# Performance work log

Measured on AMD Instinct MI355X. Metric: run time of the kernel, lower is better.

Reference implementation:

```python
import jax, jax.numpy as jnp
import numpy as np

NUM_QUERIES = 256  # num_queries init arg
D = 256            # decoder_dim


def fps(xyz, n):
    """Furthest point sampling, matching the CUDA furthest_point_sample kernel:
    start at index 0, keep running min squared distance, pick argmax each step.
    xyz: [B, N, 3] -> indices [B, n] int32."""
    B, N, _ = xyz.shape

    def step(carry, _):
        dist, far = carry
        centroid = jnp.take_along_axis(xyz, far[:, None, None], axis=1)  # [B,1,3]
        d = jnp.sum((xyz - centroid) ** 2, axis=-1)                      # [B,N]
        dist = jnp.minimum(dist, d)
        return (dist, jnp.argmax(dist, axis=-1).astype(jnp.int32)), far

    init = (jnp.full((B, N), 1e10, xyz.dtype), jnp.zeros((B,), jnp.int32))
    _, inds = jax.lax.scan(step, init, None, length=n)
    return jnp.transpose(inds)  # [B, n]


def setup_inputs() -> dict:
    key = jax.random.key(0)
    ks = jax.random.split(key, 6)
    B, N = 64, 32768
    # scene coords in roughly [-3, 3]^3 meters
    encoder_xyz = jax.random.uniform(ks[0], (B, N, 3), jnp.float32) * 6.0 - 3.0
    pc_min = jnp.min(encoder_xyz, axis=1)  # [B,3]
    pc_max = jnp.max(encoder_xyz, axis=1)  # [B,3]
    gauss_B = jax.random.normal(ks[1], (3, D // 2), jnp.float32)  # fourier freqs
    W1 = jax.random.normal(ks[2], (D, D), jnp.float32) / np.sqrt(D)
    b1 = jnp.zeros((D,), jnp.float32)
    W2 = jax.random.normal(ks[3], (D, D), jnp.float32) / np.sqrt(D)
    b2 = jnp.zeros((D,), jnp.float32)
    return dict(encoder_xyz=encoder_xyz, pc_min=pc_min, pc_max=pc_max,
                gauss_B=gauss_B, W1=W1, b1=b1, W2=W2, b2=b2)


def reference(encoder_xyz, pc_min, pc_max, gauss_B, W1, b1, W2, b2):
    # --- query selection: FPS + gather (indices are non-differentiable) ---
    inds = fps(jax.lax.stop_gradient(encoder_xyz), NUM_QUERIES)          # [B,nq]
    query_xyz = jnp.take_along_axis(encoder_xyz, inds[..., None], axis=1)  # [B,nq,3]
    # --- PositionEmbeddingCoordsSine (fourier, normalize=True) ---
    norm = (query_xyz - pc_min[:, None, :]) / (pc_max - pc_min)[:, None, :]
    proj = (2.0 * jnp.pi) * jnp.einsum('bnd,df->bnf', norm, gauss_B)     # [B,nq,D/2]
    pos = jnp.concatenate([jnp.sin(proj), jnp.cos(proj)], axis=-1)       # [B,nq,D]
    pos = jnp.transpose(pos, (0, 2, 1))                                   # [B,D,nq]
    # --- query_projection GenericMLP: conv1x1 + ReLU, conv1x1 + output ReLU ---
    h = jax.nn.relu(jnp.einsum('bcn,dc->bdn', pos, W1) + b1[:, None])
    query_embed = jax.nn.relu(jnp.einsum('bcn,dc->bdn', h, W2) + b2[:, None])
    return query_xyz, query_embed
```

## Files before the change

kernel.cpp:

```cpp
#include <hip/hip_runtime.h>

#define FPS_N 32768
#define FPS_T 256
#define NBLK 8
#define PPB (FPS_N / NBLK)
#define PPT (PPB / FPS_T)
#define NCH (PPT / 4)
#define NQ 256
#define DD 256
#define NT 64
#define B_BATCH 64

#define WS_CLEAR_BYTES (B_BATCH * NQ * NBLK * 8)

__global__ __attribute__((amdgpu_flat_work_group_size(FPS_T, FPS_T),
                          amdgpu_waves_per_eu(2, 2)))
void fps_kernel(const float* __restrict__ xyz, float* __restrict__ qout,
                unsigned long long* __restrict__ gslot) {
  const int gid = blockIdx.x;
  const int xcd = gid & 7;
  const int s = gid >> 3;
  const int b = xcd + 8 * (s >> 3);
  const int q = s & 7;
  const int t = threadIdx.x;

  const float* __restrict__ base = xyz + (size_t)b * (FPS_N * 3);
  const float4* __restrict__ base4 =
      (const float4*)(base + (size_t)q * PPB * 3) + (size_t)t * (PPT * 3 / 4);
  float* qb = qout + (size_t)b * (NQ * 3);
  unsigned long long* bslot = gslot + (size_t)b * (NQ * NBLK);

  __shared__ unsigned long long sred[FPS_T / 64];
  __shared__ float4 bc;

  float4 C[PPT * 3 / 4];
#pragma unroll
  for (int i = 0; i < PPT * 3 / 4; ++i) C[i] = base4[i];
#pragma unroll
  for (int i = 0; i < PPT * 3 / 4; ++i) {
    asm volatile("" : "+v"(C[i].x), "+v"(C[i].y), "+v"(C[i].z), "+v"(C[i].w));
  }
  float4 Dst[NCH];
#pragma unroll
  for (int c = 0; c < NCH; ++c) Dst[c] = make_float4(1e10f, 1e10f, 1e10f, 1e10f);

  if (q == 0 && t == 0) { qb[0] = base[0]; qb[1] = base[1]; qb[2] = base[2]; }
  float cx = base[0], cy = base[1], cz = base[2];

#pragma unroll 1
  for (int j = 1; j < NQ; ++j) {
    float best = -1.0f;
    int bik = 0;

#pragma unroll
    for (int c = 0; c < NCH; ++c) {
      const float4 a4 = C[3 * c + 0];
      const float4 b4 = C[3 * c + 1];
      const float4 c4 = C[3 * c + 2];
      const float px[4] = {a4.x, a4.w, b4.z, c4.y};
      const float py[4] = {a4.y, b4.x, b4.w, c4.z};
      const float pz[4] = {a4.z, b4.y, c4.x, c4.w};
      const float dold[4] = {Dst[c].x, Dst[c].y, Dst[c].z, Dst[c].w};
      float dnew[4];
#pragma unroll
      for (int i = 0; i < 4; ++i) {
        const float dx = __fsub_rn(px[i], cx);
        const float dy = __fsub_rn(py[i], cy);
        const float dz = __fsub_rn(pz[i], cz);
        const float d = __fadd_rn(__fadd_rn(__fmul_rn(dx, dx), __fmul_rn(dy, dy)),
                                  __fmul_rn(dz, dz));
        const float nd = fminf(dold[i], d);
        dnew[i] = nd;
        if (nd > best) { best = nd; bik = c * 4 + i; }
      }
      Dst[c] = make_float4(dnew[0], dnew[1], dnew[2], dnew[3]);
    }
    int bi = q * PPB + t * PPT + bik;

#pragma unroll
    for (int off = 32; off; off >>= 1) {
      const float ov = __shfl_xor(best, off);
      const int oi = __shfl_xor(bi, off);
      if (ov > best || (ov == best && oi < bi)) { best = ov; bi = oi; }
    }
    if ((t & 63) == 0) {
      sred[t >> 6] = ((unsigned long long)(unsigned int)__float_as_int(best) << 32) |
                     (unsigned int)~(unsigned int)bi;
    }
    __syncthreads();

    if (t < 64) {
      unsigned long long p = sred[t & 3];
#pragma unroll
      for (int off = 1; off < 4; off <<= 1) {
        const unsigned long long o = __shfl_xor(p, off);
        if (o > p) p = o;
      }
      if (t == 0) {
        __hip_atomic_store(&bslot[j * NBLK + q], p, __ATOMIC_RELAXED,
                           __HIP_MEMORY_SCOPE_AGENT);
      }
      unsigned long long rp = 0;
      if (t < NBLK) {
        do {
          rp = __hip_atomic_load(&bslot[j * NBLK + t], __ATOMIC_RELAXED,
                                 __HIP_MEMORY_SCOPE_AGENT);
        } while (rp == 0ull);
      }
#pragma unroll
      for (int off = 1; off < NBLK; off <<= 1) {
        const unsigned long long o = __shfl_xor(rp, off);
        if (o > rp) rp = o;
      }
      if (t == 0) {
        const int gi = (int)~(unsigned int)(rp & 0xffffffffull);
        const float* cp = base + 3 * (size_t)gi;
        const float ncx = cp[0], ncy = cp[1], ncz = cp[2];
        bc = make_float4(ncx, ncy, ncz, 0.f);
        if (q == 0) { qb[3 * j + 0] = ncx; qb[3 * j + 1] = ncy; qb[3 * j + 2] = ncz; }
      }
    }
    __syncthreads();
    cx = bc.x; cy = bc.y; cz = bc.z;
  }
}

__global__ __launch_bounds__(256) void embed_mlp_kernel(
    const float* __restrict__ qxyz, const float* __restrict__ pcmin,
    const float* __restrict__ pcmax, const float* __restrict__ G,
    const float* __restrict__ W1, const float* __restrict__ b1,
    const float* __restrict__ W2, const float* __restrict__ b2,
    float* __restrict__ out) {
  const int b = blockIdx.x >> 2;
  const int n0 = (blockIdx.x & 3) * NT;
  const int tid = threadIdx.x;
  const int ty = tid >> 4, tx = tid & 15;

  __shared__ __align__(16) float P[DD][NT + 4];
  __shared__ __align__(16) float H[DD][NT + 4];
  __shared__ __align__(16) float Wl[64][NT + 4];
  __shared__ float snorm[NT][3];

  if (tid < NT) {
    const int n = n0 + tid;
    const float qx = qxyz[(size_t)b * (NQ * 3) + 3 * n + 0];
    const float qy = qxyz[(size_t)b * (NQ * 3) + 3 * n + 1];
    const float qz = qxyz[(size_t)b * (NQ * 3) + 3 * n + 2];
    snorm[tid][0] = (qx - pcmin[3 * b + 0]) / (pcmax[3 * b + 0] - pcmin[3 * b + 0]);
    snorm[tid][1] = (qy - pcmin[3 * b + 1]) / (pcmax[3 * b + 1] - pcmin[3 * b + 1]);
    snorm[tid][2] = (qz - pcmin[3 * b + 2]) / (pcmax[3 * b + 2] - pcmin[3 * b + 2]);
  }
  __syncthreads();

  {
    const int nn = tid & 63;
    const int fg = tid >> 6;
    const float nx = snorm[nn][0], ny = snorm[nn][1], nz = snorm[nn][2];
#pragma unroll 4
    for (int ff = 0; ff < 32; ++ff) {
      const int f = fg * 32 + ff;
      const float s = nx * G[f] + ny * G[128 + f] + nz * G[256 + f];
      const float proj = 6.28318530717958647692f * s;
      P[f][nn] = sinf(proj);
      P[f + 128][nn] = cosf(proj);
    }
  }

  for (int layer = 0; layer < 2; ++layer) {
    const float* W = layer ? W2 : W1;
    const float* bias = layer ? b2 : b1;
    const float (*src)[NT + 4] = layer ? H : P;

    for (int dt = 0; dt < 4; ++dt) {
      float acc[4][4] = {};
      for (int kt = 0; kt < 4; ++kt) {
        __syncthreads();
        {
          const int r = tid >> 2;
          const int cb = (tid & 3) * 16;
          const float* wrow = W + (size_t)(dt * 64 + r) * DD + kt * 64 + cb;
#pragma unroll
          for (int i = 0; i < 4; ++i) {
            const float4 v = *(const float4*)(wrow + 4 * i);
            Wl[cb + 4 * i + 0][r] = v.x;
            Wl[cb + 4 * i + 1][r] = v.y;
            Wl[cb + 4 * i + 2][r] = v.z;
            Wl[cb + 4 * i + 3][r] = v.w;
          }
        }
        __syncthreads();
#pragma unroll 8
        for (int cc = 0; cc < 64; ++cc) {
          const float4 a = *(const float4*)&Wl[cc][ty * 4];
          const float4 p4 = *(const float4*)&src[kt * 64 + cc][tx * 4];
          acc[0][0] = fmaf(a.x, p4.x, acc[0][0]);
          acc[0][1] = fmaf(a.x, p4.y, acc[0][1]);
          acc[0][2] = fmaf(a.x, p4.z, acc[0][2]);
          acc[0][3] = fmaf(a.x, p4.w, acc[0][3]);
          acc[1][0] = fmaf(a.y, p4.x, acc[1][0]);
          acc[1][1] = fmaf(a.y, p4.y, acc[1][1]);
          acc[1][2] = fmaf(a.y, p4.z, acc[1][2]);
          acc[1][3] = fmaf(a.y, p4.w, acc[1][3]);
          acc[2][0] = fmaf(a.z, p4.x, acc[2][0]);
          acc[2][1] = fmaf(a.z, p4.y, acc[2][1]);
          acc[2][2] = fmaf(a.z, p4.z, acc[2][2]);
          acc[2][3] = fmaf(a.z, p4.w, acc[2][3]);
          acc[3][0] = fmaf(a.w, p4.x, acc[3][0]);
          acc[3][1] = fmaf(a.w, p4.y, acc[3][1]);
          acc[3][2] = fmaf(a.w, p4.z, acc[3][2]);
          acc[3][3] = fmaf(a.w, p4.w, acc[3][3]);
        }
      }
      if (layer == 0) {
#pragma unroll
        for (int i = 0; i < 4; ++i) {
          const float bv = bias[dt * 64 + ty * 4 + i];
          float4 h;
          h.x = fmaxf(acc[i][0] + bv, 0.f);
          h.y = fmaxf(acc[i][1] + bv, 0.f);
          h.z = fmaxf(acc[i][2] + bv, 0.f);
          h.w = fmaxf(acc[i][3] + bv, 0.f);
          *(float4*)&H[dt * 64 + ty * 4 + i][tx * 4] = h;
        }
      } else {
        float* ob = out + (size_t)b * (DD * NQ);
#pragma unroll
        for (int i = 0; i < 4; ++i) {
          const float bv = bias[dt * 64 + ty * 4 + i];
          float4 h;
          h.x = fmaxf(acc[i][0] + bv, 0.f);
          h.y = fmaxf(acc[i][1] + bv, 0.f);
          h.z = fmaxf(acc[i][2] + bv, 0.f);
          h.w = fmaxf(acc[i][3] + bv, 0.f);
          *(float4*)(ob + (size_t)(dt * 64 + ty * 4 + i) * NQ + n0 + tx * 4) = h;
        }
      }
    }
  }
}

extern "C" void kernel_launch(void* const* d_in, const int* in_sizes, int n_in,
                              void* d_out, int out_size, void* d_ws, size_t ws_size,
                              hipStream_t stream) {
  (void)in_sizes; (void)n_in; (void)ws_size; (void)out_size;
  const float* xyz   = (const float*)d_in[0];
  const float* pcmin = (const float*)d_in[1];
  const float* pcmax = (const float*)d_in[2];
  const float* G     = (const float*)d_in[3];
  const float* W1    = (const float*)d_in[4];
  const float* b1    = (const float*)d_in[5];
  const float* W2    = (const float*)d_in[6];
  const float* b2    = (const float*)d_in[7];

  float* qxyz  = (float*)d_out;
  float* embed = qxyz + (size_t)B_BATCH * NQ * 3;

  unsigned long long* gslot = (unsigned long long*)d_ws;

  hipMemsetAsync(d_ws, 0, WS_CLEAR_BYTES, stream);

  hipLaunchKernelGGL(fps_kernel, dim3(B_BATCH * NBLK), dim3(FPS_T), 0, stream,
                     xyz, qxyz, gslot);
  hipLaunchKernelGGL(embed_mlp_kernel, dim3(B_BATCH * 4), dim3(256), 0, stream,
                     qxyz, pcmin, pcmax, G, W1, b1, W2, b2, embed);
}
```

Before: 582.4 us.

## Carry winning point coordinates through FPS reductions to skip global centroid reload

Each thread now selects the coordinates of its best point from registers and carries them, along with the packed distance/index key, through the wave, block and cross-block reductions. Each block publishes three 64-bit slots (key, xy, z) instead of one. The final lane then reads the centroid from the reduced values rather than loading it from global memory after the reduction, taking a dependent global load off the serial per-iteration critical path. In exchange it adds register selection work, extra shuffles and triple the slot traffic, and switches the ready sentinel to all-ones with a 0xFF memset.

```diff
diff --git a/kernel.cpp b/kernel.cpp
--- a/kernel.cpp
+++ b/kernel.cpp
@@ -11,7 +11,8 @@
 #define NT 64
 #define B_BATCH 64
 
-#define WS_CLEAR_BYTES (B_BATCH * NQ * NBLK * 8)
+#define WS_CLEAR_BYTES (B_BATCH * NQ * NBLK * 3 * 8)
+#define SENT 0xffffffffffffffffull
 
 __global__ __attribute__((amdgpu_flat_work_group_size(FPS_T, FPS_T),
                           amdgpu_waves_per_eu(2, 2)))
@@ -23,14 +24,17 @@
   const int b = xcd + 8 * (s >> 3);
   const int q = s & 7;
   const int t = threadIdx.x;
+  const int w = t >> 6;
+  const int lane = t & 63;
 
   const float* __restrict__ base = xyz + (size_t)b * (FPS_N * 3);
   const float4* __restrict__ base4 =
       (const float4*)(base + (size_t)q * PPB * 3) + (size_t)t * (PPT * 3 / 4);
   float* qb = qout + (size_t)b * (NQ * 3);
-  unsigned long long* bslot = gslot + (size_t)b * (NQ * NBLK);
-
-  __shared__ unsigned long long sred[FPS_T / 64];
+  unsigned long long* bslot = gslot + ((size_t)b * NQ) * (NBLK * 3);
+
+  __shared__ unsigned long long redp[FPS_T / 64], redxy[FPS_T / 64];
+  __shared__ float redz[FPS_T / 64];
   __shared__ float4 bc;
 
   float4 C[PPT * 3 / 4];
@@ -75,49 +79,81 @@
       }
       Dst[c] = make_float4(dnew[0], dnew[1], dnew[2], dnew[3]);
     }
-    int bi = q * PPB + t * PPT + bik;
+    const int bi = q * PPB + t * PPT + bik;
+    unsigned long long p =
+        ((unsigned long long)(unsigned int)__float_as_int(best) << 32) |
+        (unsigned int)~(unsigned int)bi;
+
+    float wx = 0.f, wy = 0.f, wz = 0.f;
+#pragma unroll
+    for (int c = 0; c < NCH; ++c) {
+      const float4 a4 = C[3 * c + 0];
+      const float4 b4 = C[3 * c + 1];
+      const float4 c4 = C[3 * c + 2];
+      const float px[4] = {a4.x, a4.w, b4.z, c4.y};
+      const float py[4] = {a4.y, b4.x, b4.w, c4.z};
+      const float pz[4] = {a4.z, b4.y, c4.x, c4.w};
+#pragma unroll
+      for (int i = 0; i < 4; ++i) {
+        if (c * 4 + i == bik) { wx = px[i]; wy = py[i]; wz = pz[i]; }
+      }
+    }
+    unsigned long long pxy = ((unsigned long long)__float_as_uint(wy) << 32) |
+                             __float_as_uint(wx);
+    float pz2 = wz;
 
 #pragma unroll
     for (int off = 32; off; off >>= 1) {
-      const float ov = __shfl_xor(best, off);
-      const int oi = __shfl_xor(bi, off);
-      if (ov > best || (ov == best && oi < bi)) { best = ov; bi = oi; }
-    }
-    if ((t & 63) == 0) {
-      sred[t >> 6] = ((unsigned long long)(unsigned int)__float_as_int(best) << 32) |
-                     (unsigned int)~(unsigned int)bi;
-    }
+      const unsigned long long op = __shfl_xor(p, off);
+      const unsigned long long oxy = __shfl_xor(pxy, off);
+      const float oz = __shfl_xor(pz2, off);
+      if (op > p) { p = op; pxy = oxy; pz2 = oz; }
+    }
+    if (lane == 0) { redp[w] = p; redxy[w] = pxy; redz[w] = pz2; }
     __syncthreads();
 
-    if (t < 64) {
-      unsigned long long p = sred[t & 3];
-#pragma unroll
-      for (int off = 1; off < 4; off <<= 1) {
-        const unsigned long long o = __shfl_xor(p, off);
-        if (o > p) p = o;
-      }
-      if (t == 0) {
-        __hip_atomic_store(&bslot[j * NBLK + q], p, __ATOMIC_RELAXED,
-                           __HIP_MEMORY_SCOPE_AGENT);
-      }
-      unsigned long long rp = 0;
-      if (t < NBLK) {
+    if (w == 0) {
+      if (lane < 4) {
+        p = redp[lane]; pxy = redxy[lane]; pz2 = redz[lane];
+#pragma unroll
+        for (int off = 1; off < 4; off <<= 1) {
+          const unsigned long long op = __shfl_xor(p, off);
+          const unsigned long long oxy = __shfl_xor(pxy, off);
+          const float oz = __shfl_xor(pz2, off);
+          if (op > p) { p = op; pxy = oxy; pz2 = oz; }
+        }
+      }
+      if (lane == 0) {
+        unsigned long long* sl = bslot + (size_t)j * (NBLK * 3) + q * 3;
+        __hip_atomic_store(&sl[0], p, __ATOMIC_RELAXED, __HIP_MEMORY_SCOPE_AGENT);
+        __hip_atomic_store(&sl[1], pxy, __ATOMIC_RELAXED, __HIP_MEMORY_SCOPE_AGENT);
+        __hip_atomic_store(&sl[2], (unsigned long long)__float_as_uint(pz2),
+                           __ATOMIC_RELAXED, __HIP_MEMORY_SCOPE_AGENT);
+      }
+      unsigned long long own = 0;
+      if (lane < NBLK * 3) {
+        const unsigned long long* sl = bslot + (size_t)j * (NBLK * 3) + lane;
         do {
-          rp = __hip_atomic_load(&bslot[j * NBLK + t], __ATOMIC_RELAXED,
-                                 __HIP_MEMORY_SCOPE_AGENT);
-        } while (rp == 0ull);
-      }
+          own = __hip_atomic_load(sl, __ATOMIC_RELAXED, __HIP_MEMORY_SCOPE_AGENT);
+        } while (own == SENT);
+      }
+      const int l3 = lane * 3;
+      const unsigned long long gp = __shfl(own, l3);
+      const unsigned long long gxy = __shfl(own, l3 + 1);
+      const unsigned long long gz = __shfl(own, l3 + 2);
+      p = gp; pxy = gxy; pz2 = __uint_as_float((unsigned int)gz);
 #pragma unroll
       for (int off = 1; off < NBLK; off <<= 1) {
-        const unsigned long long o = __shfl_xor(rp, off);
-        if (o > rp) rp = o;
-      }
-      if (t == 0) {
-        const int gi = (int)~(unsigned int)(rp & 0xffffffffull);
-        const float* cp = base + 3 * (size_t)gi;
-        const float ncx = cp[0], ncy = cp[1], ncz = cp[2];
-        bc = make_float4(ncx, ncy, ncz, 0.f);
-        if (q == 0) { qb[3 * j + 0] = ncx; qb[3 * j + 1] = ncy; qb[3 * j + 2] = ncz; }
+        const unsigned long long op = __shfl_xor(p, off);
+        const unsigned long long oxy = __shfl_xor(pxy, off);
+        const float oz = __shfl_xor(pz2, off);
+        if (op > p) { p = op; pxy = oxy; pz2 = oz; }
+      }
+      if (lane == 0) {
+        const float ncx = __uint_as_float((unsigned int)(pxy & 0xffffffffull));
+        const float ncy = __uint_as_float((unsigned int)(pxy >> 32));
+        bc = make_float4(ncx, ncy, pz2, 0.f);
+        if (q == 0) { qb[3 * j + 0] = ncx; qb[3 * j + 1] = ncy; qb[3 * j + 2] = pz2; }
       }
     }
     __syncthreads();
@@ -257,7 +293,7 @@
 
   unsigned long long* gslot = (unsigned long long*)d_ws;
 
-  hipMemsetAsync(d_ws, 0, WS_CLEAR_BYTES, stream);
+  hipMemsetAsync(d_ws, 0xFF, WS_CLEAR_BYTES, stream);
 
   hipLaunchKernelGGL(fps_kernel, dim3(B_BATCH * NBLK), dim3(FPS_T), 0, stream,
                      xyz, qxyz, gslot);
```

Result: slower. 759.0 us (+30.3%).

## Drop second barrier per FPS step by having every wave poll cross-block slots

Applied to the files above, without the earlier changes.

Each FPS iteration now performs the intra-block reduction with a single packed 64-bit shuffle and a double-buffered shared slot. All four waves then redundantly do the final block combine and spin on the global per-block slots, and each loads the new centroid directly. This removes the second __syncthreads and the LDS broadcast of the centroid. The workspace sentinel changes from zero to all-ones so that a real packed value can never match it. The trade-off is four times as many polling loads on the global slots and redundant centroid loads per block.

```diff
diff --git a/kernel.cpp b/kernel.cpp
--- a/kernel.cpp
+++ b/kernel.cpp
@@ -12,6 +12,7 @@
 #define B_BATCH 64
 
 #define WS_CLEAR_BYTES (B_BATCH * NQ * NBLK * 8)
+#define SENT 0xffffffffffffffffull
 
 __global__ __attribute__((amdgpu_flat_work_group_size(FPS_T, FPS_T),
                           amdgpu_waves_per_eu(2, 2)))
@@ -23,6 +24,8 @@
   const int b = xcd + 8 * (s >> 3);
   const int q = s & 7;
   const int t = threadIdx.x;
+  const int w = t >> 6;
+  const int lane = t & 63;
 
   const float* __restrict__ base = xyz + (size_t)b * (FPS_N * 3);
   const float4* __restrict__ base4 =
@@ -30,8 +33,7 @@
   float* qb = qout + (size_t)b * (NQ * 3);
   unsigned long long* bslot = gslot + (size_t)b * (NQ * NBLK);
 
-  __shared__ unsigned long long sred[FPS_T / 64];
-  __shared__ float4 bc;
+  __shared__ unsigned long long sredp[2][4];
 
   float4 C[PPT * 3 / 4];
 #pragma unroll
@@ -75,53 +77,52 @@
       }
       Dst[c] = make_float4(dnew[0], dnew[1], dnew[2], dnew[3]);
     }
-    int bi = q * PPB + t * PPT + bik;
+    const int bi = q * PPB + t * PPT + bik;
+    unsigned long long p =
+        ((unsigned long long)(unsigned int)__float_as_int(best) << 32) |
+        (unsigned int)~(unsigned int)bi;
 
 #pragma unroll
     for (int off = 32; off; off >>= 1) {
-      const float ov = __shfl_xor(best, off);
-      const int oi = __shfl_xor(bi, off);
-      if (ov > best || (ov == best && oi < bi)) { best = ov; bi = oi; }
-    }
-    if ((t & 63) == 0) {
-      sred[t >> 6] = ((unsigned long long)(unsigned int)__float_as_int(best) << 32) |
-                     (unsigned int)~(unsigned int)bi;
-    }
+      const unsigned long long o = __shfl_xor(p, off);
+      if (o > p) p = o;
+    }
+    if (lane == 0) sredp[j & 1][w] = p;
     __syncthreads();
 
-    if (t < 64) {
-      unsigned long long p = sred[t & 3];
-#pragma unroll
-      for (int off = 1; off < 4; off <<= 1) {
-        const unsigned long long o = __shfl_xor(p, off);
-        if (o > p) p = o;
-      }
-      if (t == 0) {
-        __hip_atomic_store(&bslot[j * NBLK + q], p, __ATOMIC_RELAXED,
-                           __HIP_MEMORY_SCOPE_AGENT);
-      }
-      unsigned long long rp = 0;
-      if (t < NBLK) {
-        do {
-          rp = __hip_atomic_load(&bslot[j * NBLK + t], __ATOMIC_RELAXED,
-                                 __HIP_MEMORY_SCOPE_AGENT);
-        } while (rp == 0ull);
-      }
-#pragma unroll
-      for (int off = 1; off < NBLK; off <<= 1) {
-        const unsigned long long o = __shfl_xor(rp, off);
-        if (o > rp) rp = o;
-      }
-      if (t == 0) {
-        const int gi = (int)~(unsigned int)(rp & 0xffffffffull);
-        const float* cp = base + 3 * (size_t)gi;
-        const float ncx = cp[0], ncy = cp[1], ncz = cp[2];
-        bc = make_float4(ncx, ncy, ncz, 0.f);
-        if (q == 0) { qb[3 * j + 0] = ncx; qb[3 * j + 1] = ncy; qb[3 * j + 2] = ncz; }
-      }
-    }
-    __syncthreads();
-    cx = bc.x; cy = bc.y; cz = bc.z;
+    unsigned long long bp = 0;
+    if (lane < 4) bp = sredp[j & 1][lane];
+#pragma unroll
+    for (int off = 1; off < 4; off <<= 1) {
+      const unsigned long long o = __shfl_xor(bp, off);
+      if (o > bp) bp = o;
+    }
+    if (w == 0 && lane == 0) {
+      __hip_atomic_store(&bslot[j * NBLK + q], bp, __ATOMIC_RELAXED,
+                         __HIP_MEMORY_SCOPE_AGENT);
+    }
+
+    unsigned long long own = SENT;
+    if (lane < NBLK) {
+      const unsigned long long* sl = &bslot[j * NBLK + lane];
+      do {
+        own = __hip_atomic_load(sl, __ATOMIC_RELAXED, __HIP_MEMORY_SCOPE_AGENT);
+      } while (own == SENT);
+    }
+#pragma unroll
+    for (int off = 1; off < NBLK; off <<= 1) {
+      const unsigned long long o = __shfl_xor(own, off);
+      if (o > own) own = o;
+    }
+    const unsigned int lo =
+        __builtin_amdgcn_readfirstlane((unsigned int)(own & 0xffffffffull));
+    const int gi = (int)~lo;
+    const float* cp = base + 3 * (size_t)gi;
+    cx = cp[0]; cy = cp[1]; cz = cp[2];
+
+    if (q == 0 && t == 0) {
+      qb[3 * j + 0] = cx; qb[3 * j + 1] = cy; qb[3 * j + 2] = cz;
+    }
   }
 }
 
@@ -257,7 +258,7 @@
 
   unsigned long long* gslot = (unsigned long long*)d_ws;
 
-  hipMemsetAsync(d_ws, 0, WS_CLEAR_BYTES, stream);
+  hipMemsetAsync(d_ws, 0xFF, WS_CLEAR_BYTES, stream);
 
   hipLaunchKernelGGL(fps_kernel, dim3(B_BATCH * NBLK), dim3(FPS_T), 0, stream,
                      xyz, qxyz, gslot);
```

After: 677.4 us. 1.16x slower.
